# Kernel tuning notes

Hardware: AMD Instinct MI355X
Metric: run time of the kernel (lower is better)

The kernel has to match this reference:

```python
import jax, jax.numpy as jnp
import numpy as np

D_CONV = 4  # matches Mamba(d_conv=4)


def _silu(v):
    return v * jax.nn.sigmoid(v)


def _mamba_block(x, in_w, cw, cb, xw, dtw, dtb, A_log, Dp, ow):
    # x: (B, L, d_model)
    B, L, _ = x.shape
    d_inner, d_state = A_log.shape
    xz = x @ in_w.T                        # (B, L, 2*d_inner)
    xr, z = jnp.split(xz, 2, axis=-1)      # each (B, L, d_inner)
    # causal depthwise conv1d (pad d_conv-1 on the left, truncate to L)
    xp = jnp.pad(xr, ((0, 0), (D_CONV - 1, 0), (0, 0)))
    xc = sum(xp[:, k:k + L, :] * cw[:, k] for k in range(D_CONV)) + cb
    xc = _silu(xc)                         # (B, L, d_inner)
    dbl = xc @ xw.T                        # (B, L, dt_rank + 2*d_state)
    dt_rank = dbl.shape[-1] - 2 * d_state
    dt, Bm, Cm = jnp.split(dbl, [dt_rank, dt_rank + d_state], axis=-1)
    dt = jax.nn.softplus(dt @ dtw.T + dtb)  # (B, L, d_inner)
    A = -jnp.exp(A_log)                    # (d_inner, d_state)
    dA = jnp.exp(dt[..., None] * A)                          # (B, L, d_inner, d_state)
    dBx = dt[..., None] * Bm[:, :, None, :] * xc[..., None]  # (B, L, d_inner, d_state)

    def step(h, inputs):
        dA_t, dBx_t, C_t = inputs          # (B,d,s), (B,d,s), (B,s)
        h = dA_t * h + dBx_t
        y = jnp.einsum('bds,bs->bd', h, C_t)
        return h, y

    h0 = jnp.zeros((B, d_inner, d_state), x.dtype)
    _, ys = jax.lax.scan(step, h0, (dA.transpose(1, 0, 2, 3),
                                    dBx.transpose(1, 0, 2, 3),
                                    Cm.transpose(1, 0, 2)))
    y = ys.transpose(1, 0, 2) + xc * Dp    # skip term D*u
    y = y * _silu(z)                       # gated
    return y @ ow.T                        # (B, L, d_model)


def setup_inputs() -> dict:
    key = jax.random.key(0)
    d_model, d_state, n_layer = 1024, 16, 2
    d_inner = 2 * d_model
    dt_rank = d_model // 16  # ceil(1024/16)
    Bsz, L = 2, 1024
    ks = jax.random.split(key, 8)
    s = 0.02
    x = jax.random.normal(ks[0], (Bsz, L, d_model), jnp.float32)
    in_proj_w = jax.random.normal(ks[1], (n_layer, 2 * d_inner, d_model), jnp.float32) * s
    conv_w = jax.random.normal(ks[2], (n_layer, d_inner, D_CONV), jnp.float32) * 0.2
    conv_b = jnp.zeros((n_layer, d_inner), jnp.float32)
    x_proj_w = jax.random.normal(ks[3], (n_layer, dt_rank + 2 * d_state, d_inner), jnp.float32) * s
    dt_proj_w = jax.random.normal(ks[4], (n_layer, d_inner, dt_rank), jnp.float32) * s
    dt_proj_b = jax.random.uniform(ks[5], (n_layer, d_inner), jnp.float32, -5.0, -3.0)
    A_log = jnp.log(jnp.tile(jnp.arange(1, d_state + 1, dtype=jnp.float32), (n_layer, d_inner, 1)))
    D = jnp.ones((n_layer, d_inner), jnp.float32)
    out_proj_w = jax.random.normal(ks[6], (n_layer, d_model, d_inner), jnp.float32) * s
    return {"x": x, "in_proj_w": in_proj_w, "conv_w": conv_w, "conv_b": conv_b,
            "x_proj_w": x_proj_w, "dt_proj_w": dt_proj_w, "dt_proj_b": dt_proj_b,
            "A_log": A_log, "D": D, "out_proj_w": out_proj_w}


def reference(x, in_proj_w, conv_w, conv_b, x_proj_w, dt_proj_w, dt_proj_b, A_log, D, out_proj_w):
    n_layer = in_proj_w.shape[0]
    for i in range(n_layer):
        x = _mamba_block(x, in_proj_w[i], conv_w[i], conv_b[i], x_proj_w[i],
                         dt_proj_w[i], dt_proj_b[i], A_log[i], D[i], out_proj_w[i])
    return x
```

## Files before the change

kernel.cpp:

```cpp
#include <hip/hip_runtime.h>
#include <hip/hip_bf16.h>
#include <cmath>

typedef __bf16 bf16x8_t __attribute__((ext_vector_type(8)));
typedef float  f32x4_t  __attribute__((ext_vector_type(4)));
using bf16 = __hip_bfloat16;

#define LOG2E 1.44269504088896340736f
#define LN2   0.69314718055994530942f

#define AS1C(p) ((const __attribute__((address_space(1))) void*)(p))
#define AS3C(p) ((__attribute__((address_space(3))) void*)(p))

__device__ __forceinline__ float fexp2(float x) { return __builtin_amdgcn_exp2f(x); }
__device__ __forceinline__ float flog2(float x) { return __builtin_amdgcn_logf(x); }
__device__ __forceinline__ float frcp (float x) { return __builtin_amdgcn_rcpf(x); }

__global__ __launch_bounds__(256)
void cast_multi(const float* s0, bf16* d0, int e0,
                const float* s1, bf16* d1, int e1,
                const float* s2, bf16* d2, int e2,
                const float* s3, bf16* d3, int e3,
                const float* s4, bf16* d4, int e4)
{
    const int blk = blockIdx.x;
    const float* src; bf16* dst; int base;
    if      (blk < e0) { src = s0; dst = d0; base = blk; }
    else if (blk < e1) { src = s1; dst = d1; base = blk - e0; }
    else if (blk < e2) { src = s2; dst = d2; base = blk - e1; }
    else if (blk < e3) { src = s3; dst = d3; base = blk - e2; }
    else               { src = s4; dst = d4; base = blk - e3; }

    const int i = base * 256 + threadIdx.x;
    const float4* s = (const float4*)(src + (size_t)i * 8);
    float4 a = s[0], b = s[1];
    bf16 o[8];
    o[0] = __float2bfloat16(a.x); o[1] = __float2bfloat16(a.y);
    o[2] = __float2bfloat16(a.z); o[3] = __float2bfloat16(a.w);
    o[4] = __float2bfloat16(b.x); o[5] = __float2bfloat16(b.y);
    o[6] = __float2bfloat16(b.z); o[7] = __float2bfloat16(b.w);
    *(int4*)(dst + (size_t)i * 8) = *(int4*)o;
}

template<int MODE, bool SPLITK>
__global__ __launch_bounds__(256)
void gemm_bf16(const bf16* __restrict__ A, const bf16* __restrict__ B,
               float* __restrict__ Cf, bf16* __restrict__ Cb,
               int M, int N, int K, int lda, int ldb, int ldc)
{
    __shared__ __align__(16) bf16 At[2][128][32];
    __shared__ __align__(16) bf16 Bt[2][128][32];

    const int tid  = threadIdx.x;
    const int lane = tid & 63;
    const int wid  = tid >> 6;
    const int wr   = wid >> 1;
    const int wc   = wid & 1;
    const int fr   = lane & 15;
    const int fq   = lane >> 4;

    const int row0 = blockIdx.y * 128;
    const int col0 = blockIdx.x * 128;
    const int kb   = SPLITK ? blockIdx.z * K : 0;

    const int g_row = wid * 32 + (lane >> 2);
    const int g_kp  = (((lane & 3) ^ ((lane >> 3) & 3)) * 8);
    const bf16* aP0 = A + (size_t)(row0 + g_row) * lda + g_kp + kb;
    const bf16* aP1 = A + (size_t)(row0 + g_row + 16) * lda + g_kp + kb;
    int bR0 = col0 + g_row;      if (bR0 >= N) bR0 = N - 1;
    int bR1 = col0 + g_row + 16; if (bR1 >= N) bR1 = N - 1;
    const bf16* bP0 = B + (size_t)bR0 * ldb + g_kp + kb;
    const bf16* bP1 = B + (size_t)bR1 * ldb + g_kp + kb;

    const int rchunk = (fq ^ ((fr >> 1) & 3)) * 8;

    f32x4_t acc[4][4];
    #pragma unroll
    for (int m = 0; m < 4; ++m)
        #pragma unroll
        for (int n = 0; n < 4; ++n)
            acc[m][n] = f32x4_t{0.f, 0.f, 0.f, 0.f};

    auto STAGE = [&](int buf, int k0) {
        __builtin_amdgcn_global_load_lds(AS1C(aP0 + k0), AS3C(&At[buf][wid * 32][0]),      16, 0, 0);
        __builtin_amdgcn_global_load_lds(AS1C(aP1 + k0), AS3C(&At[buf][wid * 32 + 16][0]), 16, 0, 0);
        __builtin_amdgcn_global_load_lds(AS1C(bP0 + k0), AS3C(&Bt[buf][wid * 32][0]),      16, 0, 0);
        __builtin_amdgcn_global_load_lds(AS1C(bP1 + k0), AS3C(&Bt[buf][wid * 32 + 16][0]), 16, 0, 0);
    };

    STAGE(0, 0);
    __syncthreads();
    int cur = 0;
    for (int k0 = 0; k0 < K; k0 += 32) {
        if (k0 + 32 < K) STAGE(cur ^ 1, k0 + 32);

        bf16x8_t af[4], bg[4];
        #pragma unroll
        for (int m = 0; m < 4; ++m)
            af[m] = *(const bf16x8_t*)&At[cur][wr * 64 + m * 16 + fr][rchunk];
        #pragma unroll
        for (int n = 0; n < 4; ++n)
            bg[n] = *(const bf16x8_t*)&Bt[cur][wc * 64 + n * 16 + fr][rchunk];
        #pragma unroll
        for (int m = 0; m < 4; ++m)
            #pragma unroll
            for (int n = 0; n < 4; ++n)
                acc[m][n] = __builtin_amdgcn_mfma_f32_16x16x32_bf16(
                    af[m], bg[n], acc[m][n], 0, 0, 0);

        __syncthreads();
        cur ^= 1;
    }

    float* Cfz = SPLITK ? (Cf + (size_t)blockIdx.z * M * ldc) : Cf;

    #pragma unroll
    for (int m = 0; m < 4; ++m) {
        #pragma unroll
        for (int n = 0; n < 4; ++n) {
            const int c = col0 + wc * 64 + n * 16 + fr;
            if (c < N) {
                #pragma unroll
                for (int r = 0; r < 4; ++r) {
                    const int rr = row0 + wr * 64 + m * 16 + fq * 4 + r;
                    if (SPLITK || MODE != 1) Cfz[(size_t)rr * ldc + c] = acc[m][n][r];
                    if (!SPLITK && MODE != 0) Cb[(size_t)rr * ldc + c] = __float2bfloat16(acc[m][n][r]);
                }
            }
        }
    }
}

__global__ __launch_bounds__(256)
void reduce_pk(const float* __restrict__ part, float* __restrict__ of,
               bf16* __restrict__ oh, int n4, int stride4, int S)
{
    const int i = blockIdx.x * blockDim.x + threadIdx.x;
    if (i >= n4) return;
    const float4* p4 = (const float4*)part;
    float4 s = p4[i];
    for (int k = 1; k < S; ++k) {
        float4 v = p4[(size_t)k * stride4 + i];
        s.x += v.x; s.y += v.y; s.z += v.z; s.w += v.w;
    }
    if (of) ((float4*)of)[i] = s;
    if (oh) {
        bf16 o[4];
        o[0] = __float2bfloat16(s.x); o[1] = __float2bfloat16(s.y);
        o[2] = __float2bfloat16(s.z); o[3] = __float2bfloat16(s.w);
        *(int2*)(oh + (size_t)i * 4) = *(int2*)o;
    }
}

__global__ __launch_bounds__(256)
void conv_silu(const bf16* __restrict__ xz, const float* __restrict__ cw,
               const float* __restrict__ cb, bf16* __restrict__ xc,
               int Bsz, int L, int dinner)
{
    const int nv = dinner / 4;
    const int g  = blockIdx.x * blockDim.x + threadIdx.x;
    const int d4 = (g % nv) * 4;
    const int t  = (g / nv) % L;
    const int b  = g / (nv * L);
    if (b >= Bsz) return;

    const int ldxz = 2 * dinner;
    float4 w0 = *(const float4*)(cw + (size_t)(d4 + 0) * 4);
    float4 w1 = *(const float4*)(cw + (size_t)(d4 + 1) * 4);
    float4 w2 = *(const float4*)(cw + (size_t)(d4 + 2) * 4);
    float4 w3 = *(const float4*)(cw + (size_t)(d4 + 3) * 4);
    float4 acc = *(const float4*)(cb + d4);

    const bf16* base = xz + (size_t)b * L * ldxz + d4;
    #pragma unroll
    for (int k = 0; k < 4; ++k) {
        const int ts = t - 3 + k;
        if (ts >= 0) {
            const bf16* rp = base + (size_t)ts * ldxz;
            float vx = __bfloat162float(rp[0]);
            float vy = __bfloat162float(rp[1]);
            float vz = __bfloat162float(rp[2]);
            float vw = __bfloat162float(rp[3]);
            acc.x = fmaf(vx, (&w0.x)[k], acc.x);
            acc.y = fmaf(vy, (&w1.x)[k], acc.y);
            acc.z = fmaf(vz, (&w2.x)[k], acc.z);
            acc.w = fmaf(vw, (&w3.x)[k], acc.w);
        }
    }
    acc.x = acc.x * frcp(1.f + fexp2(-acc.x * LOG2E));
    acc.y = acc.y * frcp(1.f + fexp2(-acc.y * LOG2E));
    acc.z = acc.z * frcp(1.f + fexp2(-acc.z * LOG2E));
    acc.w = acc.w * frcp(1.f + fexp2(-acc.w * LOG2E));

    bf16 o[4];
    o[0] = __float2bfloat16(acc.x); o[1] = __float2bfloat16(acc.y);
    o[2] = __float2bfloat16(acc.z); o[3] = __float2bfloat16(acc.w);
    *(int2*)(xc + ((size_t)b * L + t) * dinner + d4) = *(int2*)o;
}

__global__ __launch_bounds__(256)
void scan_part1(const bf16* __restrict__ dtraw, const bf16* __restrict__ xc,
                const float* __restrict__ dbl, const float* __restrict__ dtb,
                const float* __restrict__ alog, float* __restrict__ hend,
                float* __restrict__ Ssum, int Bsz, int L, int dinner,
                int NC, int CL)
{
    const int g  = blockIdx.x * blockDim.x + threadIdx.x;
    const int sq = g & 3;
    const int d  = (g >> 2) % dinner;
    const int c  = ((g >> 2) / dinner) % NC;
    const int b  = g / (4 * dinner * NC);
    if (b >= Bsz) return;

    float4 av = *(const float4*)(alog + (size_t)d * 16 + sq * 4);
    const float As0 = -fexp2(av.x * LOG2E) * LOG2E;
    const float As1 = -fexp2(av.y * LOG2E) * LOG2E;
    const float As2 = -fexp2(av.z * LOG2E) * LOG2E;
    const float As3 = -fexp2(av.w * LOG2E) * LOG2E;
    const float bias = dtb[d];

    const int t0 = c * CL;
    const bf16*  dt_p = dtraw + ((size_t)b * L + t0) * dinner + d;
    const bf16*  xc_p = xc    + ((size_t)b * L + t0) * dinner + d;
    const float* bl_p = dbl   + ((size_t)b * L + t0) * 96 + 64 + sq * 4;

    float h0 = 0.f, h1 = 0.f, h2 = 0.f, h3 = 0.f, S = 0.f;
    for (int t = 0; t < CL; ++t) {
        const float dtv = __bfloat162float(*dt_p);
        const float xcv = __bfloat162float(*xc_p);
        const float4 Bv = *(const float4*)bl_p;

        const float xv = dtv + bias;
        const float e  = fexp2(xv * LOG2E);
        const float sp = (xv > 15.f) ? xv : LN2 * flog2(1.f + e);
        S += sp;
        const float u = sp * xcv;
        h0 = fmaf(fexp2(sp * As0), h0, u * Bv.x);
        h1 = fmaf(fexp2(sp * As1), h1, u * Bv.y);
        h2 = fmaf(fexp2(sp * As2), h2, u * Bv.z);
        h3 = fmaf(fexp2(sp * As3), h3, u * Bv.w);

        dt_p += dinner; xc_p += dinner; bl_p += 96;
    }

    const size_t idx = ((size_t)b * NC + c) * dinner + d;
    *(float4*)(hend + idx * 16 + sq * 4) = make_float4(h0, h1, h2, h3);
    if (sq == 0) Ssum[idx] = S;
}

__global__ __launch_bounds__(256)
void chunk_prefix(float* __restrict__ hend, const float* __restrict__ Ssum,
                  const float* __restrict__ alog, int Bsz, int dinner, int NC)
{
    const int g = blockIdx.x * blockDim.x + threadIdx.x;
    const int s = g & 15;
    const int d = (g >> 4) % dinner;
    const int b = g / (16 * dinner);
    if (b >= Bsz) return;

    const float As2 = -fexp2(alog[(size_t)d * 16 + s] * LOG2E) * LOG2E;

    float h = 0.f;
    for (int c = 0; c < NC; ++c) {
        const size_t idx = ((size_t)b * NC + c) * dinner + d;
        const float he = hend[idx * 16 + s];
        const float Sv = Ssum[idx];
        hend[idx * 16 + s] = h;
        h = fmaf(fexp2(As2 * Sv), h, he);
    }
}

__global__ __launch_bounds__(256)
void scan_part2(bf16* dty, const bf16* __restrict__ xc,
                const float* __restrict__ dbl, const bf16* __restrict__ xz,
                const float* __restrict__ dtb, const float* __restrict__ alog,
                const float* __restrict__ Dp, const float* __restrict__ hinit,
                int Bsz, int L, int dinner, int NC, int CL)
{
    const int g  = blockIdx.x * blockDim.x + threadIdx.x;
    const int sq = g & 3;
    const int d  = (g >> 2) % dinner;
    const int c  = ((g >> 2) / dinner) % NC;
    const int b  = g / (4 * dinner * NC);
    if (b >= Bsz) return;

    float4 av = *(const float4*)(alog + (size_t)d * 16 + sq * 4);
    const float As0 = -fexp2(av.x * LOG2E) * LOG2E;
    const float As1 = -fexp2(av.y * LOG2E) * LOG2E;
    const float As2 = -fexp2(av.z * LOG2E) * LOG2E;
    const float As3 = -fexp2(av.w * LOG2E) * LOG2E;
    const float bias = dtb[d];
    const float Dval = Dp[d];

    const size_t cidx = ((size_t)b * NC + c) * dinner + d;
    float4 hv = *(const float4*)(hinit + cidx * 16 + sq * 4);
    float h0 = hv.x, h1 = hv.y, h2 = hv.z, h3 = hv.w;

    const int t0 = c * CL;
    bf16*        dt_p = dty + ((size_t)b * L + t0) * dinner + d;
    const bf16*  xc_p = xc  + ((size_t)b * L + t0) * dinner + d;
    const float* bl_p = dbl + ((size_t)b * L + t0) * 96 + 64 + sq * 4;
    const bf16*  z_p  = xz  + ((size_t)b * L + t0) * (2 * dinner) + dinner + d;

    for (int t = 0; t < CL; ++t) {
        const float dtv = __bfloat162float(*dt_p);
        const float xcv = __bfloat162float(*xc_p);
        const float4 Bv = *(const float4*)bl_p;
        const float4 Cv = *(const float4*)(bl_p + 16);
        const float zv  = __bfloat162float(*z_p);

        const float xv = dtv + bias;
        const float e  = fexp2(xv * LOG2E);
        const float sp = (xv > 15.f) ? xv : LN2 * flog2(1.f + e);
        const float u = sp * xcv;
        h0 = fmaf(fexp2(sp * As0), h0, u * Bv.x);
        h1 = fmaf(fexp2(sp * As1), h1, u * Bv.y);
        h2 = fmaf(fexp2(sp * As2), h2, u * Bv.z);
        h3 = fmaf(fexp2(sp * As3), h3, u * Bv.w);

        float y = h0 * Cv.x + h1 * Cv.y + h2 * Cv.z + h3 * Cv.w;
        y += __shfl_xor(y, 1, 4);
        y += __shfl_xor(y, 2, 4);

        if (sq == 0) {
            y = fmaf(xcv, Dval, y);
            const float sig = frcp(1.f + fexp2(-zv * LOG2E));
            *dt_p = __float2bfloat16(y * (zv * sig));
        }

        dt_p += dinner; xc_p += dinner; bl_p += 96; z_p += 2 * dinner;
    }
}

extern "C" void kernel_launch(void* const* d_in, const int* in_sizes, int n_in,
                              void* d_out, int out_size, void* d_ws, size_t ws_size,
                              hipStream_t stream)
{
    const float* x    = (const float*)d_in[0];
    const float* inw  = (const float*)d_in[1];
    const float* cw   = (const float*)d_in[2];
    const float* cb   = (const float*)d_in[3];
    const float* xw   = (const float*)d_in[4];
    const float* dtw  = (const float*)d_in[5];
    const float* dtb  = (const float*)d_in[6];
    const float* alog = (const float*)d_in[7];
    const float* Dp   = (const float*)d_in[8];
    const float* ow   = (const float*)d_in[9];
    float* out = (float*)d_out;

    const int Bsz = 2, L = 1024, dmodel = 1024, dinner = 2048;
    const int BL = Bsz * L;
    const int NC = 32, CL = L / NC;
    const int SPX = 16, KSX = dinner / SPX;
    const int SPO = 2,  KSO = dinner / SPO;

    char* p = (char*)d_ws;
    auto alloc = [&](size_t bytes) { char* r = p; p += (bytes + 63) & ~size_t(63); return r; };
    bf16*  wb_in  = (bf16*) alloc((size_t)2 * 2 * dinner * dmodel * 2);
    bf16*  wb_x   = (bf16*) alloc((size_t)2 * 96 * dinner * 2);
    bf16*  wb_dt  = (bf16*) alloc((size_t)2 * dinner * 64 * 2);
    bf16*  wb_ow  = (bf16*) alloc((size_t)2 * dmodel * dinner * 2);
    bf16*  curb   = (bf16*) alloc((size_t)BL * dmodel * 2);
    bf16*  xzb16  = (bf16*) alloc((size_t)BL * 2 * dinner * 2);
    bf16*  xcb16  = (bf16*) alloc((size_t)BL * dinner * 2);
    float* dblb   = (float*)alloc((size_t)BL * 96 * 4);
    bf16*  dblb16 = (bf16*) alloc((size_t)BL * 96 * 2);
    bf16*  dtrb16 = (bf16*) alloc((size_t)BL * dinner * 2);
    float* hendb  = (float*)alloc((size_t)Bsz * NC * dinner * 16 * 4);
    float* ssumb  = (float*)alloc((size_t)Bsz * NC * dinner * 4);
    float* partb  = (float*)alloc((size_t)SPO * BL * dmodel * 4);

    const int scan_blocks = (Bsz * NC * dinner * 4) / 256;
    const int pfx_blocks  = (Bsz * dinner * 16) / 256;

    {
        const int n8_x  = BL * dmodel / 8;
        const int n8_in = 2 * 2 * dinner * dmodel / 8;
        const int n8_xw = 2 * 96 * dinner / 8;
        const int n8_dt = 2 * dinner * 64 / 8;
        const int n8_ow = 2 * dmodel * dinner / 8;
        const int e0 = n8_x / 256;
        const int e1 = e0 + n8_in / 256;
        const int e2 = e1 + n8_xw / 256;
        const int e3 = e2 + n8_dt / 256;
        const int e4 = e3 + n8_ow / 256;
        cast_multi<<<e4, 256, 0, stream>>>(
            x, curb, e0, inw, wb_in, e1, xw, wb_x, e2, dtw, wb_dt, e3, ow, wb_ow, e4);
    }

    for (int l = 0; l < 2; ++l) {
        const bf16*  wb_in_l = wb_in + (size_t)l * 2 * dinner * dmodel;
        const bf16*  wb_x_l  = wb_x  + (size_t)l * 96 * dinner;
        const bf16*  wb_dt_l = wb_dt + (size_t)l * dinner * 64;
        const bf16*  wb_ow_l = wb_ow + (size_t)l * dmodel * dinner;
        const float* cw_l    = cw   + (size_t)l * dinner * 4;
        const float* cb_l    = cb   + (size_t)l * dinner;
        const float* dtb_l   = dtb  + (size_t)l * dinner;
        const float* alog_l  = alog + (size_t)l * dinner * 16;
        const float* Dp_l    = Dp   + (size_t)l * dinner;

        gemm_bf16<1, false><<<dim3(2 * dinner / 128, BL / 128), 256, 0, stream>>>(
            curb, wb_in_l, nullptr, xzb16, BL, 2 * dinner, dmodel, dmodel, dmodel, 2 * dinner);

        conv_silu<<<(BL * dinner / 4) / 256, 256, 0, stream>>>(
            xzb16, cw_l, cb_l, xcb16, Bsz, L, dinner);

        gemm_bf16<0, true><<<dim3(1, BL / 128, SPX), 256, 0, stream>>>(
            xcb16, wb_x_l, partb, nullptr, BL, 96, KSX, dinner, dinner, 96);
        reduce_pk<<<(BL * 96 / 4 + 255) / 256, 256, 0, stream>>>(
            partb, dblb, dblb16, BL * 96 / 4, BL * 96 / 4, SPX);

        gemm_bf16<1, false><<<dim3(dinner / 128, BL / 128), 256, 0, stream>>>(
            dblb16, wb_dt_l, nullptr, dtrb16, BL, dinner, 64, 96, 64, dinner);

        scan_part1<<<scan_blocks, 256, 0, stream>>>(
            dtrb16, xcb16, dblb, dtb_l, alog_l, hendb, ssumb, Bsz, L, dinner, NC, CL);
        chunk_prefix<<<pfx_blocks, 256, 0, stream>>>(
            hendb, ssumb, alog_l, Bsz, dinner, NC);
        scan_part2<<<scan_blocks, 256, 0, stream>>>(
            dtrb16, xcb16, dblb, xzb16, dtb_l, alog_l, Dp_l, hendb,
            Bsz, L, dinner, NC, CL);

        gemm_bf16<0, true><<<dim3(dmodel / 128, BL / 128, SPO), 256, 0, stream>>>(
            dtrb16, wb_ow_l, partb, nullptr, BL, dmodel, KSO, dinner, dinner, dmodel);
        if (l == 0)
            reduce_pk<<<(BL * dmodel / 4 + 255) / 256, 256, 0, stream>>>(
                partb, nullptr, curb, BL * dmodel / 4, BL * dmodel / 4, SPO);
        else
            reduce_pk<<<(BL * dmodel / 4 + 255) / 256, 256, 0, stream>>>(
                partb, out, nullptr, BL * dmodel / 4, BL * dmodel / 4, SPO);
    }
}
```

Measured before the change: 332.6 us.

## Give each scan thread all 16 states and double the chunk count

The chunked selective-scan kernels now assign one thread to one (batch, chunk, channel) holding all 16 state values, instead of four threads of four states each. This drops the cross-lane shuffle reduction and the four-fold repeated softplus, dt, x and z loads, at the cost of more registers per thread. Chunk count goes from 32 to 64 so the thread count stays high with shorter per-chunk loops. The chunk-end state buffer now aliases the out-projection partial buffer, which relies on that buffer being unused while the scan runs.

```diff
diff --git a/kernel.cpp b/kernel.cpp
--- a/kernel.cpp
+++ b/kernel.cpp
@@ -205,47 +205,61 @@
                 float* __restrict__ Ssum, int Bsz, int L, int dinner,
                 int NC, int CL)
 {
-    const int g  = blockIdx.x * blockDim.x + threadIdx.x;
-    const int sq = g & 3;
-    const int d  = (g >> 2) % dinner;
-    const int c  = ((g >> 2) / dinner) % NC;
-    const int b  = g / (4 * dinner * NC);
+    const int g = blockIdx.x * blockDim.x + threadIdx.x;
+    const int d = g % dinner;
+    const int c = (g / dinner) % NC;
+    const int b = g / (dinner * NC);
     if (b >= Bsz) return;
 
-    float4 av = *(const float4*)(alog + (size_t)d * 16 + sq * 4);
-    const float As0 = -fexp2(av.x * LOG2E) * LOG2E;
-    const float As1 = -fexp2(av.y * LOG2E) * LOG2E;
-    const float As2 = -fexp2(av.z * LOG2E) * LOG2E;
-    const float As3 = -fexp2(av.w * LOG2E) * LOG2E;
+    const float* ap = alog + (size_t)d * 16;
+    float a_[16];
+    *(float4*)&a_[0]  = *(const float4*)(ap + 0);
+    *(float4*)&a_[4]  = *(const float4*)(ap + 4);
+    *(float4*)&a_[8]  = *(const float4*)(ap + 8);
+    *(float4*)&a_[12] = *(const float4*)(ap + 12);
+    float As[16];
+    #pragma unroll
+    for (int i = 0; i < 16; ++i) As[i] = -fexp2(a_[i] * LOG2E) * LOG2E;
     const float bias = dtb[d];
 
     const int t0 = c * CL;
     const bf16*  dt_p = dtraw + ((size_t)b * L + t0) * dinner + d;
     const bf16*  xc_p = xc    + ((size_t)b * L + t0) * dinner + d;
-    const float* bl_p = dbl   + ((size_t)b * L + t0) * 96 + 64 + sq * 4;
-
-    float h0 = 0.f, h1 = 0.f, h2 = 0.f, h3 = 0.f, S = 0.f;
+    const float* bl_p = dbl   + ((size_t)b * L + t0) * 96 + 64;
+
+    float h[16];
+    #pragma unroll
+    for (int i = 0; i < 16; ++i) h[i] = 0.f;
+    float S = 0.f;
+
     for (int t = 0; t < CL; ++t) {
         const float dtv = __bfloat162float(*dt_p);
         const float xcv = __bfloat162float(*xc_p);
-        const float4 Bv = *(const float4*)bl_p;
+        float Bv[16];
+        *(float4*)&Bv[0]  = *(const float4*)(bl_p + 0);
+        *(float4*)&Bv[4]  = *(const float4*)(bl_p + 4);
+        *(float4*)&Bv[8]  = *(const float4*)(bl_p + 8);
+        *(float4*)&Bv[12] = *(const float4*)(bl_p + 12);
 
         const float xv = dtv + bias;
         const float e  = fexp2(xv * LOG2E);
         const float sp = (xv > 15.f) ? xv : LN2 * flog2(1.f + e);
         S += sp;
         const float u = sp * xcv;
-        h0 = fmaf(fexp2(sp * As0), h0, u * Bv.x);
-        h1 = fmaf(fexp2(sp * As1), h1, u * Bv.y);
-        h2 = fmaf(fexp2(sp * As2), h2, u * Bv.z);
-        h3 = fmaf(fexp2(sp * As3), h3, u * Bv.w);
+        #pragma unroll
+        for (int i = 0; i < 16; ++i)
+            h[i] = fmaf(fexp2(sp * As[i]), h[i], u * Bv[i]);
 
         dt_p += dinner; xc_p += dinner; bl_p += 96;
     }
 
     const size_t idx = ((size_t)b * NC + c) * dinner + d;
-    *(float4*)(hend + idx * 16 + sq * 4) = make_float4(h0, h1, h2, h3);
-    if (sq == 0) Ssum[idx] = S;
+    float* hp = hend + idx * 16;
+    *(float4*)(hp + 0)  = make_float4(h[0],  h[1],  h[2],  h[3]);
+    *(float4*)(hp + 4)  = make_float4(h[4],  h[5],  h[6],  h[7]);
+    *(float4*)(hp + 8)  = make_float4(h[8],  h[9],  h[10], h[11]);
+    *(float4*)(hp + 12) = make_float4(h[12], h[13], h[14], h[15]);
+    Ssum[idx] = S;
 }
 
 __global__ __launch_bounds__(256)
@@ -277,56 +291,66 @@
                 const float* __restrict__ Dp, const float* __restrict__ hinit,
                 int Bsz, int L, int dinner, int NC, int CL)
 {
-    const int g  = blockIdx.x * blockDim.x + threadIdx.x;
-    const int sq = g & 3;
-    const int d  = (g >> 2) % dinner;
-    const int c  = ((g >> 2) / dinner) % NC;
-    const int b  = g / (4 * dinner * NC);
+    const int g = blockIdx.x * blockDim.x + threadIdx.x;
+    const int d = g % dinner;
+    const int c = (g / dinner) % NC;
+    const int b = g / (dinner * NC);
     if (b >= Bsz) return;
 
-    float4 av = *(const float4*)(alog + (size_t)d * 16 + sq * 4);
-    const float As0 = -fexp2(av.x * LOG2E) * LOG2E;
-    const float As1 = -fexp2(av.y * LOG2E) * LOG2E;
-    const float As2 = -fexp2(av.z * LOG2E) * LOG2E;
-    const float As3 = -fexp2(av.w * LOG2E) * LOG2E;
+    const float* ap = alog + (size_t)d * 16;
+    float a_[16];
+    *(float4*)&a_[0]  = *(const float4*)(ap + 0);
+    *(float4*)&a_[4]  = *(const float4*)(ap + 4);
+    *(float4*)&a_[8]  = *(const float4*)(ap + 8);
+    *(float4*)&a_[12] = *(const float4*)(ap + 12);
+    float As[16];
+    #pragma unroll
+    for (int i = 0; i < 16; ++i) As[i] = -fexp2(a_[i] * LOG2E) * LOG2E;
     const float bias = dtb[d];
     const float Dval = Dp[d];
 
     const size_t cidx = ((size_t)b * NC + c) * dinner + d;
-    float4 hv = *(const float4*)(hinit + cidx * 16 + sq * 4);
-    float h0 = hv.x, h1 = hv.y, h2 = hv.z, h3 = hv.w;
+    float h[16];
+    const float* hp = hinit + cidx * 16;
+    *(float4*)&h[0]  = *(const float4*)(hp + 0);
+    *(float4*)&h[4]  = *(const float4*)(hp + 4);
+    *(float4*)&h[8]  = *(const float4*)(hp + 8);
+    *(float4*)&h[12] = *(const float4*)(hp + 12);
 
     const int t0 = c * CL;
     bf16*        dt_p = dty + ((size_t)b * L + t0) * dinner + d;
     const bf16*  xc_p = xc  + ((size_t)b * L + t0) * dinner + d;
-    const float* bl_p = dbl + ((size_t)b * L + t0) * 96 + 64 + sq * 4;
+    const float* bl_p = dbl + ((size_t)b * L + t0) * 96 + 64;
     const bf16*  z_p  = xz  + ((size_t)b * L + t0) * (2 * dinner) + dinner + d;
 
     for (int t = 0; t < CL; ++t) {
         const float dtv = __bfloat162float(*dt_p);
         const float xcv = __bfloat162float(*xc_p);
-        const float4 Bv = *(const float4*)bl_p;
-        const float4 Cv = *(const float4*)(bl_p + 16);
         const float zv  = __bfloat162float(*z_p);
+        float Bv[16], Cv[16];
+        *(float4*)&Bv[0]  = *(const float4*)(bl_p + 0);
+        *(float4*)&Bv[4]  = *(const float4*)(bl_p + 4);
+        *(float4*)&Bv[8]  = *(const float4*)(bl_p + 8);
+        *(float4*)&Bv[12] = *(const float4*)(bl_p + 12);
+        *(float4*)&Cv[0]  = *(const float4*)(bl_p + 16);
+        *(float4*)&Cv[4]  = *(const float4*)(bl_p + 20);
+        *(float4*)&Cv[8]  = *(const float4*)(bl_p + 24);
+        *(float4*)&Cv[12] = *(const float4*)(bl_p + 28);
 
         const float xv = dtv + bias;
         const float e  = fexp2(xv * LOG2E);
         const float sp = (xv > 15.f) ? xv : LN2 * flog2(1.f + e);
         const float u = sp * xcv;
-        h0 = fmaf(fexp2(sp * As0), h0, u * Bv.x);
-        h1 = fmaf(fexp2(sp * As1), h1, u * Bv.y);
-        h2 = fmaf(fexp2(sp * As2), h2, u * Bv.z);
-        h3 = fmaf(fexp2(sp * As3), h3, u * Bv.w);
-
-        float y = h0 * Cv.x + h1 * Cv.y + h2 * Cv.z + h3 * Cv.w;
-        y += __shfl_xor(y, 1, 4);
-        y += __shfl_xor(y, 2, 4);
-
-        if (sq == 0) {
-            y = fmaf(xcv, Dval, y);
-            const float sig = frcp(1.f + fexp2(-zv * LOG2E));
-            *dt_p = __float2bfloat16(y * (zv * sig));
+        float y = 0.f;
+        #pragma unroll
+        for (int i = 0; i < 16; ++i) {
+            h[i] = fmaf(fexp2(sp * As[i]), h[i], u * Bv[i]);
+            y = fmaf(h[i], Cv[i], y);
         }
+
+        y = fmaf(xcv, Dval, y);
+        const float sig = frcp(1.f + fexp2(-zv * LOG2E));
+        *dt_p = __float2bfloat16(y * (zv * sig));
 
         dt_p += dinner; xc_p += dinner; bl_p += 96; z_p += 2 * dinner;
     }
@@ -350,7 +374,7 @@
 
     const int Bsz = 2, L = 1024, dmodel = 1024, dinner = 2048;
     const int BL = Bsz * L;
-    const int NC = 32, CL = L / NC;
+    const int NC = 64, CL = L / NC;
     const int SPX = 16, KSX = dinner / SPX;
     const int SPO = 2,  KSO = dinner / SPO;
 
@@ -366,11 +390,11 @@
     float* dblb   = (float*)alloc((size_t)BL * 96 * 4);
     bf16*  dblb16 = (bf16*) alloc((size_t)BL * 96 * 2);
     bf16*  dtrb16 = (bf16*) alloc((size_t)BL * dinner * 2);
-    float* hendb  = (float*)alloc((size_t)Bsz * NC * dinner * 16 * 4);
     float* ssumb  = (float*)alloc((size_t)Bsz * NC * dinner * 4);
     float* partb  = (float*)alloc((size_t)SPO * BL * dmodel * 4);
-
-    const int scan_blocks = (Bsz * NC * dinner * 4) / 256;
+    float* hendb  = partb;
+
+    const int scan_blocks = (Bsz * NC * dinner) / 256;
     const int pfx_blocks  = (Bsz * dinner * 16) / 256;
 
     {
```

Result: no change. 333.9 us (+0.4%).
